# Performance work log

Measured on AMD Instinct MI355X. Metric: run time of the kernel, lower is better.

## Reference

```python
import jax, jax.numpy as jnp
import numpy as np

NUM_PARAMS = 1024
BATCH = 65536


def build_lifted_core(rotation_params, diagonal_scaling_params, n):
    """Faithful translation of the torch forward's lifted-core construction."""
    h = n // 2
    dt = rotation_params.dtype
    # skew-symmetric matrix S[i,j] = r[i] - r[j]
    S = rotation_params[:, None] - rotation_params[None, :]
    I = jnp.eye(h, dtype=dt)
    # Cayley transform: (I - S)^{-1} (I + S)
    rotation = jnp.linalg.solve(I - S, I + S)
    # core = diag(d) @ rotation  (row scaling)
    core = diagonal_scaling_params[:, None] * rotation  # [h, h]
    # rot90 has period 4 in k -> precompute the 4 distinct rotated cores
    rots = jnp.stack([jnp.rot90(core, k=k) for k in range(4)])  # [4, h, h]

    def body(o, L):
        blk = jax.lax.dynamic_slice(L, (o, o), (h, h)) + rots[o % 4]
        return jax.lax.dynamic_update_slice(L, blk, (o, o))

    lifted = jax.lax.fori_loop(0, h + 1, body, jnp.zeros((n, n), dtype=dt))
    return lifted


def setup_inputs() -> dict:
    key = jax.random.key(0)
    k1, k2, k3 = jax.random.split(key, 3)
    x = jax.random.normal(k1, (BATCH, NUM_PARAMS), dtype=jnp.float32)
    rotation_params = jax.random.normal(k2, (NUM_PARAMS // 2,), dtype=jnp.float32)
    diagonal_scaling_params = jax.random.normal(k3, (NUM_PARAMS // 2,), dtype=jnp.float32)
    return {"x": x, "rotation_params": rotation_params,
            "diagonal_scaling_params": diagonal_scaling_params}


def reference(x, rotation_params, diagonal_scaling_params):
    n = x.shape[-1]
    lifted = build_lifted_core(rotation_params, diagonal_scaling_params, n)
    return x @ lifted.T
```

## Files before the change

kernel.cpp:

```cpp
#include <hip/hip_runtime.h>
#include <hip/hip_bf16.h>
#include <hip/hip_fp16.h>

typedef __attribute__((ext_vector_type(8))) _Float16 h8;
typedef __attribute__((ext_vector_type(4))) float f32x4;
typedef unsigned short u16;
typedef unsigned int u32;

#define GLOAD16(g, l)                                                          \
  __builtin_amdgcn_global_load_lds((const __attribute__((address_space(1))) u32*)(g), \
                                   (__attribute__((address_space(3))) u32*)(l), 16, 0, 0)

__global__ __launch_bounds__(512) void prep_kernel(const float* __restrict__ r,
                                                   const float* __restrict__ d,
                                                   float* __restrict__ pq) {
  int t = threadIdx.x;
  float rv = r[t], dv = d[t];
  float s1 = rv, s2 = rv * rv;
#pragma unroll
  for (int off = 32; off; off >>= 1) {
    s1 += __shfl_down(s1, off);
    s2 += __shfl_down(s2, off);
  }
  __shared__ float a1[8], a2[8];
  if ((t & 63) == 0) { a1[t >> 6] = s1; a2[t >> 6] = s2; }
  __syncthreads();
  float S1 = 0.f, S2 = 0.f;
#pragma unroll
  for (int w = 0; w < 8; ++w) { S1 += a1[w]; S2 += a2[w]; }
  float delta = 1.f - S1 * S1 + 512.f * S2;
  float c = 2.f / delta;
  pq[t]       = c * dv * ((1.f + S1) * rv - S2);
  pq[512 + t] = -c * dv * (512.f * rv + 1.f - S1);
}

__global__ __launch_bounds__(256) void build_lifted_diag(const float* __restrict__ rg,
                                                         const float* __restrict__ dg,
                                                         const float* __restrict__ pq,
                                                         u16* __restrict__ Lhi,
                                                         u16* __restrict__ Llo) {
  __shared__ float r_s[512], d_s[512];
  __shared__ float W[6][512];
  const int t = threadIdx.x;
  const int delta = (int)blockIdx.x - 1023;
#pragma unroll
  for (int u = 0; u < 2; ++u) {
    int a = t + (u << 8);
    r_s[a] = rg[a];
    d_s[a] = dg[a];
    W[0][a] = pq[a];
  }
  __syncthreads();
#pragma unroll
  for (int u = 0; u < 2; ++u) {
    int a = t + (u << 8);
    float qa = pq[512 + a];
    W[1][a] = d_s[a];
    int ap = a + delta, am = a - delta;
    int bp = 511 + delta - a, bm = 511 - delta - a;
    W[2][a] = ((unsigned)ap < 512u) ? qa * r_s[ap] : 0.f;
    W[3][a] = ((unsigned)am < 512u) ? qa * r_s[am] : 0.f;
    W[4][a] = ((unsigned)bp < 512u) ? qa * r_s[bp] : 0.f;
    W[5][a] = ((unsigned)bm < 512u) ? qa * r_s[bm] : 0.f;
  }
  __syncthreads();
  float* Wf = &W[0][0];
  for (int s = 4; s <= 256; s <<= 1) {
    float tmp[12];
#pragma unroll
    for (int u = 0; u < 12; ++u) {
      int idx = t + (u << 8);
      tmp[u] = ((idx & 511) >= s) ? Wf[idx - s] : 0.f;
    }
    __syncthreads();
#pragma unroll
    for (int u = 0; u < 12; ++u) Wf[t + (u << 8)] += tmp[u];
    __syncthreads();
  }
  const float* Pp = W[0]; const float* Pd = W[1];
  const float* CP = W[2]; const float* CM = W[3];
  const float* DP = W[4]; const float* DM = W[5];
  const int imin = max(0, -delta), imax = min(1023, 1023 - delta);
  for (int i = imin + t; i <= imax; i += 256) {
    const int j = i + delta;
    const int olo = max(0, max(i, j) - 511);
    const int ohi = min(min(i, j), 512);
    float val = 0.f;
    {
      int oc = olo + ((0 - olo) & 3);
      if (oc <= ohi) {
        int ohc = ohi - ((ohi - oc) & 3);
        int alo = i - ohc, ahi = i - oc;
        val += Pp[ahi] + CP[ahi];
        if (alo >= 4) val -= Pp[alo - 4] + CP[alo - 4];
        if (delta == 0) { val += Pd[ahi]; if (alo >= 4) val -= Pd[alo - 4]; }
      }
    }
    {
      int oc = olo + ((1 - olo) & 3);
      if (oc <= ohi) {
        int ohc = ohi - ((ohi - oc) & 3);
        int alo = j - ohc, ahi = j - oc;
        val += Pp[ahi] + DP[ahi];
        if (alo >= 4) val -= Pp[alo - 4] + DP[alo - 4];
      }
    }
    {
      int oc = olo + ((2 - olo) & 3);
      if (oc <= ohi) {
        int ohc = ohi - ((ohi - oc) & 3);
        int alo = 511 - i + oc, ahi = 511 - i + ohc;
        val += Pp[ahi] + CM[ahi];
        if (alo >= 4) val -= Pp[alo - 4] + CM[alo - 4];
        if (delta == 0) { val += Pd[ahi]; if (alo >= 4) val -= Pd[alo - 4]; }
      }
    }
    {
      int oc = olo + ((3 - olo) & 3);
      if (oc <= ohi) {
        int ohc = ohi - ((ohi - oc) & 3);
        int alo = 511 - j + oc, ahi = 511 - j + ohc;
        val += Pp[ahi] + DM[ahi];
        if (alo >= 4) val -= Pp[alo - 4] + DM[alo - 4];
      }
    }
    if (delta & 1) {
      int os = (i + j - 511) >> 1;
      if (os >= olo && os <= ohi) {
        int c = os & 3;
        if (c == 1) val += d_s[j - os];
        else if (c == 3) val += d_s[i - os];
      }
    }
    __half h = __float2half(val);
    float hf = __half2float(h);
    __half l = __float2half(val - hf);
    size_t idx = ((size_t)((i >> 7) * 16 + (j >> 6)) << 13) +
                 (size_t)((i & 127) << 6) + (size_t)((j & 63) ^ ((i & 7) << 3));
    Lhi[idx] = __half_as_ushort(h);
    Llo[idx] = __half_as_ushort(l);
  }
}

__global__ __launch_bounds__(256, 3) void gemm_kernel(const float* __restrict__ x,
                                                      const u16* __restrict__ Bhg,
                                                      const u16* __restrict__ Blg,
                                                      float* __restrict__ out) {
  __shared__ u16 Ah[8192], Bh[8192], Bl[8192];
  const int tid = threadIdx.x;
  const int nb = blockIdx.x & 7;
  const int mb = blockIdx.x >> 3;
  const int m0 = mb << 7;
  const int n0 = nb << 7;
  const int lane = tid & 63;
  const int wave = tid >> 6;
  const int wm = wave >> 1, wn = wave & 1;
  const int lr = lane & 15, lg = lane >> 4;
  const int sel = (lr & 7) << 3;

  const int srow = tid >> 4;
  const int scol = (tid & 15) << 2;
  const int sidx0 = (srow << 6) + (scol ^ ((srow & 7) << 3));
  const float* xbase = x + (size_t)(m0 + srow) * 1024 + scol;

  f32x4 acc[4][4] = {};
  int baseA[4], baseB[4];
#pragma unroll
  for (int f = 0; f < 4; ++f) {
    baseA[f] = ((wm << 6) + (f << 4) + lr) << 6;
    baseB[f] = ((wn << 6) + (f << 4) + lr) << 6;
  }
  const u16* tBh = Bhg + ((size_t)nb << 17);
  const u16* tBl = Blg + ((size_t)nb << 17);

  for (int kt = 0; kt < 16; ++kt) {
    __syncthreads();
    {
      const u16* gh = tBh + (kt << 13) + (tid << 3);
      const u16* gl = tBl + (kt << 13) + (tid << 3);
#pragma unroll
      for (int c = 0; c < 4; ++c) {
        GLOAD16(gh + (c << 11), &Bh[(tid << 3) + (c << 11)]);
        GLOAD16(gl + (c << 11), &Bl[(tid << 3) + (c << 11)]);
      }
    }
    float4 av[8];
    const float* xp = xbase + (kt << 6);
#pragma unroll
    for (int cc = 0; cc < 8; ++cc)
      av[cc] = *reinterpret_cast<const float4*>(xp + (size_t)cc * 16 * 1024);
#pragma unroll
    for (int cc = 0; cc < 8; ++cc) {
      float4 v = av[cc];
      union { __half2 h2[2]; uint2 u; } pk;
      pk.h2[0] = __floats2half2_rn(v.x, v.y);
      pk.h2[1] = __floats2half2_rn(v.z, v.w);
      *reinterpret_cast<uint2*>(&Ah[sidx0 + (cc << 10)]) = pk.u;
    }
    __syncthreads();
#pragma unroll
    for (int ks = 0; ks < 2; ++ks) {
      const int co = ((ks << 5) + (lg << 3)) ^ sel;
      h8 ah[4], bh[4], bl[4];
#pragma unroll
      for (int f = 0; f < 4; ++f) {
        ah[f] = *reinterpret_cast<const h8*>(&Ah[baseA[f] + co]);
        bh[f] = *reinterpret_cast<const h8*>(&Bh[baseB[f] + co]);
        bl[f] = *reinterpret_cast<const h8*>(&Bl[baseB[f] + co]);
      }
#pragma unroll
      for (int fm = 0; fm < 4; ++fm)
#pragma unroll
        for (int fn = 0; fn < 4; ++fn) {
          acc[fm][fn] = __builtin_amdgcn_mfma_f32_16x16x32_f16(ah[fm], bh[fn], acc[fm][fn], 0, 0, 0);
          acc[fm][fn] = __builtin_amdgcn_mfma_f32_16x16x32_f16(ah[fm], bl[fn], acc[fm][fn], 0, 0, 0);
        }
    }
  }
#pragma unroll
  for (int fm = 0; fm < 4; ++fm) {
    int row = m0 + (wm << 6) + (fm << 4) + (lg << 2);
#pragma unroll
    for (int fn = 0; fn < 4; ++fn) {
      int col = n0 + (wn << 6) + (fn << 4) + lr;
      float* op = out + (size_t)row * 1024 + col;
#pragma unroll
      for (int rr = 0; rr < 4; ++rr) op[(size_t)rr * 1024] = acc[fm][fn][rr];
    }
  }
}

extern "C" void kernel_launch(void* const* d_in, const int* in_sizes, int n_in,
                              void* d_out, int out_size, void* d_ws, size_t ws_size,
                              hipStream_t stream) {
  (void)in_sizes; (void)n_in; (void)out_size; (void)ws_size;
  const float* x  = (const float*)d_in[0];
  const float* r  = (const float*)d_in[1];
  const float* dg = (const float*)d_in[2];
  float* out = (float*)d_out;
  float* pq = (float*)d_ws;
  u16* Lhi = (u16*)((char*)d_ws + 4096);
  u16* Llo = Lhi + 1024 * 1024;

  prep_kernel<<<1, 512, 0, stream>>>(r, dg, pq);
  build_lifted_diag<<<2047, 256, 0, stream>>>(r, dg, pq, Lhi, Llo);
  gemm_kernel<<<4096, 256, 0, stream>>>(x, Lhi, Llo, out);
}
```

Before: 663.1 us.

## Pre-convert x to fp16 tiles and use double-buffered async-load GEMM

Adds a separate kernel that converts x to fp16 in a pre-swizzled tiled layout, processed in four row chunks so the fp16 scratch buffer stays small and can be reused. The GEMM is rewritten with 256x128 tiles, 512 threads and double-buffered LDS filled by direct global-to-LDS loads for both A and B, with explicit waitcnt and barriers plus setprio around the MFMA bursts. The goal is to move the A conversion out of the GEMM inner loop and overlap loads with compute. The cost is an extra pass that writes and rereads x in fp16, and eight kernel launches instead of one GEMM launch.

```diff
diff --git a/kernel.cpp b/kernel.cpp
--- a/kernel.cpp
+++ b/kernel.cpp
@@ -46,9 +46,7 @@
 #pragma unroll
   for (int u = 0; u < 2; ++u) {
     int a = t + (u << 8);
-    r_s[a] = rg[a];
-    d_s[a] = dg[a];
-    W[0][a] = pq[a];
+    r_s[a] = rg[a]; d_s[a] = dg[a]; W[0][a] = pq[a];
   }
   __syncthreads();
 #pragma unroll
@@ -142,87 +140,157 @@
   }
 }
 
-__global__ __launch_bounds__(256, 3) void gemm_kernel(const float* __restrict__ x,
-                                                      const u16* __restrict__ Bhg,
-                                                      const u16* __restrict__ Blg,
-                                                      float* __restrict__ out) {
-  __shared__ u16 Ah[8192], Bh[8192], Bl[8192];
+__global__ __launch_bounds__(256) void xcvt_kernel(const float* __restrict__ x,
+                                                   u16* __restrict__ xh) {
+  const int tid = blockIdx.x * 256 + threadIdx.x;
+  const int tile = tid >> 11;
+  const int inner = (tid << 4) & 32767;
+  const int r = inner >> 7;
+  const int coff = ((inner & 127) ^ ((r & 7) << 4)) >> 1;
+  const int mloc = tile >> 4, kt = tile & 15;
+  const float* src = x + (size_t)(mloc * 256 + r) * 1024 + kt * 64 + coff;
+  float4 v0 = *reinterpret_cast<const float4*>(src);
+  float4 v1 = *reinterpret_cast<const float4*>(src + 4);
+  union { __half2 h[4]; uint4 u; } pk;
+  pk.h[0] = __floats2half2_rn(v0.x, v0.y);
+  pk.h[1] = __floats2half2_rn(v0.z, v0.w);
+  pk.h[2] = __floats2half2_rn(v1.x, v1.y);
+  pk.h[3] = __floats2half2_rn(v1.z, v1.w);
+  *reinterpret_cast<uint4*>(xh + ((size_t)tid << 3)) = pk.u;
+}
+
+__global__ __launch_bounds__(512, 2) void gemm2_kernel(const u16* __restrict__ Axh,
+                                                       const u16* __restrict__ Lh,
+                                                       const u16* __restrict__ Ll,
+                                                       float* __restrict__ out) {
+  __shared__ u16 Abuf[2][16384];
+  __shared__ u16 Hbuf[2][8192];
+  __shared__ u16 Lbuf[2][8192];
   const int tid = threadIdx.x;
   const int nb = blockIdx.x & 7;
-  const int mb = blockIdx.x >> 3;
-  const int m0 = mb << 7;
-  const int n0 = nb << 7;
+  const int mloc = blockIdx.x >> 3;
   const int lane = tid & 63;
   const int wave = tid >> 6;
-  const int wm = wave >> 1, wn = wave & 1;
+  const int wm = wave >> 2, wn = wave & 3;
   const int lr = lane & 15, lg = lane >> 4;
   const int sel = (lr & 7) << 3;
-
-  const int srow = tid >> 4;
-  const int scol = (tid & 15) << 2;
-  const int sidx0 = (srow << 6) + (scol ^ ((srow & 7) << 3));
-  const float* xbase = x + (size_t)(m0 + srow) * 1024 + scol;
-
-  f32x4 acc[4][4] = {};
-  int baseA[4], baseB[4];
-#pragma unroll
-  for (int f = 0; f < 4; ++f) {
-    baseA[f] = ((wm << 6) + (f << 4) + lr) << 6;
-    baseB[f] = ((wn << 6) + (f << 4) + lr) << 6;
-  }
-  const u16* tBh = Bhg + ((size_t)nb << 17);
-  const u16* tBl = Blg + ((size_t)nb << 17);
-
-  for (int kt = 0; kt < 16; ++kt) {
-    __syncthreads();
-    {
-      const u16* gh = tBh + (kt << 13) + (tid << 3);
-      const u16* gl = tBl + (kt << 13) + (tid << 3);
-#pragma unroll
-      for (int c = 0; c < 4; ++c) {
-        GLOAD16(gh + (c << 11), &Bh[(tid << 3) + (c << 11)]);
-        GLOAD16(gl + (c << 11), &Bl[(tid << 3) + (c << 11)]);
-      }
-    }
-    float4 av[8];
-    const float* xp = xbase + (kt << 6);
-#pragma unroll
-    for (int cc = 0; cc < 8; ++cc)
-      av[cc] = *reinterpret_cast<const float4*>(xp + (size_t)cc * 16 * 1024);
-#pragma unroll
-    for (int cc = 0; cc < 8; ++cc) {
-      float4 v = av[cc];
-      union { __half2 h2[2]; uint2 u; } pk;
-      pk.h2[0] = __floats2half2_rn(v.x, v.y);
-      pk.h2[1] = __floats2half2_rn(v.z, v.w);
-      *reinterpret_cast<uint2*>(&Ah[sidx0 + (cc << 10)]) = pk.u;
-    }
-    __syncthreads();
-#pragma unroll
-    for (int ks = 0; ks < 2; ++ks) {
-      const int co = ((ks << 5) + (lg << 3)) ^ sel;
-      h8 ah[4], bh[4], bl[4];
-#pragma unroll
-      for (int f = 0; f < 4; ++f) {
-        ah[f] = *reinterpret_cast<const h8*>(&Ah[baseA[f] + co]);
-        bh[f] = *reinterpret_cast<const h8*>(&Bh[baseB[f] + co]);
-        bl[f] = *reinterpret_cast<const h8*>(&Bl[baseB[f] + co]);
-      }
-#pragma unroll
-      for (int fm = 0; fm < 4; ++fm)
-#pragma unroll
-        for (int fn = 0; fn < 4; ++fn) {
-          acc[fm][fn] = __builtin_amdgcn_mfma_f32_16x16x32_f16(ah[fm], bh[fn], acc[fm][fn], 0, 0, 0);
-          acc[fm][fn] = __builtin_amdgcn_mfma_f32_16x16x32_f16(ah[fm], bl[fn], acc[fm][fn], 0, 0, 0);
-        }
-    }
-  }
-#pragma unroll
-  for (int fm = 0; fm < 4; ++fm) {
-    int row = m0 + (wm << 6) + (fm << 4) + (lg << 2);
-#pragma unroll
-    for (int fn = 0; fn < 4; ++fn) {
-      int col = n0 + (wn << 6) + (fn << 4) + lr;
+  const int co0 = (lg << 3) ^ sel;
+  const int co1 = (32 + (lg << 3)) ^ sel;
+
+  int aOff[8], bOff[2];
+#pragma unroll
+  for (int f = 0; f < 8; ++f) aOff[f] = ((wm << 7) + (f << 4) + lr) << 6;
+#pragma unroll
+  for (int f = 0; f < 2; ++f) bOff[f] = ((wn << 5) + (f << 4) + lr) << 6;
+
+  const u16* gA = Axh + ((size_t)mloc << 18) + (tid << 3);
+  const u16* gH = Lh + ((size_t)nb << 17) + (tid << 3);
+  const u16* gL = Ll + ((size_t)nb << 17) + (tid << 3);
+
+#define STAGE(c, kt_) do {                                                     \
+    const u16* sa = gA + ((kt_) << 14);                                        \
+    const u16* sh = gH + ((kt_) << 13);                                        \
+    const u16* sl = gL + ((kt_) << 13);                                        \
+    GLOAD16(sa,          &Abuf[c][tid << 3]);                                  \
+    GLOAD16(sa + 4096,   &Abuf[c][(tid << 3) + 4096]);                         \
+    GLOAD16(sa + 8192,   &Abuf[c][(tid << 3) + 8192]);                         \
+    GLOAD16(sa + 12288,  &Abuf[c][(tid << 3) + 12288]);                        \
+    GLOAD16(sh,          &Hbuf[c][tid << 3]);                                  \
+    GLOAD16(sh + 4096,   &Hbuf[c][(tid << 3) + 4096]);                         \
+    GLOAD16(sl,          &Lbuf[c][tid << 3]);                                  \
+    GLOAD16(sl + 4096,   &Lbuf[c][(tid << 3) + 4096]);                         \
+  } while (0)
+
+  f32x4 acc[8][2] = {};
+
+  STAGE(0, 0);
+  STAGE(1, 1);
+  asm volatile("s_waitcnt vmcnt(8)" ::: "memory");
+  __builtin_amdgcn_s_barrier();
+  __builtin_amdgcn_sched_barrier(0);
+
+  for (int t = 0; t < 16; ++t) {
+    const int c = t & 1;
+    const u16* Ab = Abuf[c];
+    const u16* Hb = Hbuf[c];
+    const u16* Lb = Lbuf[c];
+    h8 aA[4], aB[4], bh0[2], bl0[2], bh1[2], bl1[2];
+#pragma unroll
+    for (int f = 0; f < 4; ++f) aA[f] = *reinterpret_cast<const h8*>(&Ab[aOff[f] + co0]);
+#pragma unroll
+    for (int f = 0; f < 2; ++f) {
+      bh0[f] = *reinterpret_cast<const h8*>(&Hb[bOff[f] + co0]);
+      bl0[f] = *reinterpret_cast<const h8*>(&Lb[bOff[f] + co0]);
+    }
+#pragma unroll
+    for (int f = 0; f < 4; ++f) aB[f] = *reinterpret_cast<const h8*>(&Ab[aOff[4 + f] + co0]);
+    __builtin_amdgcn_s_setprio(1);
+#pragma unroll
+    for (int f = 0; f < 4; ++f) {
+      acc[f][0] = __builtin_amdgcn_mfma_f32_16x16x32_f16(aA[f], bh0[0], acc[f][0], 0, 0, 0);
+      acc[f][0] = __builtin_amdgcn_mfma_f32_16x16x32_f16(aA[f], bl0[0], acc[f][0], 0, 0, 0);
+      acc[f][1] = __builtin_amdgcn_mfma_f32_16x16x32_f16(aA[f], bh0[1], acc[f][1], 0, 0, 0);
+      acc[f][1] = __builtin_amdgcn_mfma_f32_16x16x32_f16(aA[f], bl0[1], acc[f][1], 0, 0, 0);
+    }
+    __builtin_amdgcn_s_setprio(0);
+    h8 aC[4];
+#pragma unroll
+    for (int f = 0; f < 4; ++f) aC[f] = *reinterpret_cast<const h8*>(&Ab[aOff[f] + co1]);
+#pragma unroll
+    for (int f = 0; f < 2; ++f) {
+      bh1[f] = *reinterpret_cast<const h8*>(&Hb[bOff[f] + co1]);
+      bl1[f] = *reinterpret_cast<const h8*>(&Lb[bOff[f] + co1]);
+    }
+    __builtin_amdgcn_s_setprio(1);
+#pragma unroll
+    for (int f = 0; f < 4; ++f) {
+      acc[4 + f][0] = __builtin_amdgcn_mfma_f32_16x16x32_f16(aB[f], bh0[0], acc[4 + f][0], 0, 0, 0);
+      acc[4 + f][0] = __builtin_amdgcn_mfma_f32_16x16x32_f16(aB[f], bl0[0], acc[4 + f][0], 0, 0, 0);
+      acc[4 + f][1] = __builtin_amdgcn_mfma_f32_16x16x32_f16(aB[f], bh0[1], acc[4 + f][1], 0, 0, 0);
+      acc[4 + f][1] = __builtin_amdgcn_mfma_f32_16x16x32_f16(aB[f], bl0[1], acc[4 + f][1], 0, 0, 0);
+    }
+    __builtin_amdgcn_s_setprio(0);
+    h8 aD[4];
+#pragma unroll
+    for (int f = 0; f < 4; ++f) aD[f] = *reinterpret_cast<const h8*>(&Ab[aOff[4 + f] + co1]);
+    __builtin_amdgcn_s_setprio(1);
+#pragma unroll
+    for (int f = 0; f < 4; ++f) {
+      acc[f][0] = __builtin_amdgcn_mfma_f32_16x16x32_f16(aC[f], bh1[0], acc[f][0], 0, 0, 0);
+      acc[f][0] = __builtin_amdgcn_mfma_f32_16x16x32_f16(aC[f], bl1[0], acc[f][0], 0, 0, 0);
+      acc[f][1] = __builtin_amdgcn_mfma_f32_16x16x32_f16(aC[f], bh1[1], acc[f][1], 0, 0, 0);
+      acc[f][1] = __builtin_amdgcn_mfma_f32_16x16x32_f16(aC[f], bl1[1], acc[f][1], 0, 0, 0);
+    }
+#pragma unroll
+    for (int f = 0; f < 4; ++f) {
+      acc[4 + f][0] = __builtin_amdgcn_mfma_f32_16x16x32_f16(aD[f], bh1[0], acc[4 + f][0], 0, 0, 0);
+      acc[4 + f][0] = __builtin_amdgcn_mfma_f32_16x16x32_f16(aD[f], bl1[0], acc[4 + f][0], 0, 0, 0);
+      acc[4 + f][1] = __builtin_amdgcn_mfma_f32_16x16x32_f16(aD[f], bh1[1], acc[4 + f][1], 0, 0, 0);
+      acc[4 + f][1] = __builtin_amdgcn_mfma_f32_16x16x32_f16(aD[f], bl1[1], acc[4 + f][1], 0, 0, 0);
+    }
+    __builtin_amdgcn_s_setprio(0);
+
+    if (t < 14) {
+      __builtin_amdgcn_s_barrier();
+      __builtin_amdgcn_sched_barrier(0);
+      STAGE(c, t + 2);
+      asm volatile("s_waitcnt vmcnt(8)" ::: "memory");
+      __builtin_amdgcn_s_barrier();
+      __builtin_amdgcn_sched_barrier(0);
+    } else if (t == 14) {
+      asm volatile("s_waitcnt vmcnt(0)" ::: "memory");
+      __builtin_amdgcn_s_barrier();
+      __builtin_amdgcn_sched_barrier(0);
+    }
+  }
+#undef STAGE
+
+#pragma unroll
+  for (int fm = 0; fm < 8; ++fm) {
+    int row = (mloc << 8) + (wm << 7) + (fm << 4) + (lg << 2);
+#pragma unroll
+    for (int fn = 0; fn < 2; ++fn) {
+      int col = (nb << 7) + (wn << 5) + (fn << 4) + lr;
       float* op = out + (size_t)row * 1024 + col;
 #pragma unroll
       for (int rr = 0; rr < 4; ++rr) op[(size_t)rr * 1024] = acc[fm][fn][rr];
@@ -241,8 +309,14 @@
   float* pq = (float*)d_ws;
   u16* Lhi = (u16*)((char*)d_ws + 4096);
   u16* Llo = Lhi + 1024 * 1024;
+  u16* xh  = Llo + 1024 * 1024;
 
   prep_kernel<<<1, 512, 0, stream>>>(r, dg, pq);
   build_lifted_diag<<<2047, 256, 0, stream>>>(r, dg, pq, Lhi, Llo);
-  gemm_kernel<<<4096, 256, 0, stream>>>(x, Lhi, Llo, out);
-}
+  for (int ch = 0; ch < 4; ++ch) {
+    const float* xc = x + (size_t)ch * 16384 * 1024;
+    float* oc = out + (size_t)ch * 16384 * 1024;
+    xcvt_kernel<<<8192, 256, 0, stream>>>(xc, xh);
+    gemm2_kernel<<<512, 512, 0, stream>>>(xh, Lhi, Llo, oc);
+  }
+}
```

Result: slower. 708.5 us (+6.9%).
